# Kernel tuning notes

Hardware: AMD Instinct MI355X
Metric: run time of the kernel (lower is better)

## Reference

```python
import jax, jax.numpy as jnp
import numpy as np
from jax import lax

GRAD_MUL = 0.1   # config.model.deform_conv_grad_mul
GN_GROUPS = 32
EPS = 1e-5


def conv1d(x, w, b, padding=1):
    # x [N,C,T], w [O,I,K], b [O]
    y = lax.conv_general_dilated(x, w, window_strides=(1,),
                                 padding=[(padding, padding)],
                                 dimension_numbers=('NCH', 'OIH', 'NCH'))
    return y + b[None, :, None]


def group_norm(x, gamma, beta):
    N, C, T = x.shape
    xg = x.reshape(N, GN_GROUPS, C // GN_GROUPS, T)
    mu = jnp.mean(xg, axis=(2, 3), keepdims=True)
    var = jnp.var(xg, axis=(2, 3), keepdims=True)
    xn = ((xg - mu) * lax.rsqrt(var + EPS)).reshape(N, C, T)
    return xn * gamma[None, :, None] + beta[None, :, None]


def deform_conv1d(x, off_y, w, b):
    # x [N,C,T]; off_y [N,3,T] per-tap temporal offsets; w [O,I,3]; b [O]
    # kernel=3, padding=1: tap k samples at t + (k-1) + off_y[:,k,t]
    N, C, T = x.shape
    K = 3
    base = jnp.arange(T, dtype=x.dtype)[None, None, :] + \
           (jnp.arange(K, dtype=x.dtype) - 1.0)[None, :, None]   # [1,3,T]
    pos = base + off_y                                           # [N,3,T]
    p0 = jnp.floor(pos)
    w1 = pos - p0                                                # linear interp weight
    i0 = p0.astype(jnp.int32)
    i1 = i0 + 1

    def gather(idx):
        valid = (idx >= 0) & (idx < T)                           # zero padding outside
        ic = jnp.clip(idx, 0, T - 1)
        idx_b = jnp.broadcast_to(ic[:, None, :, :], (N, C, K, T))
        x_b = jnp.broadcast_to(x[:, :, None, :], (N, C, K, T))
        g = jnp.take_along_axis(x_b, idx_b, axis=3)              # [N,C,3,T]
        return g * valid[:, None, :, :].astype(x.dtype)

    sampled = gather(i0) * (1.0 - w1)[:, None] + gather(i1) * w1[:, None]  # [N,C,3,T]
    return jnp.einsum('oik,nikt->not', w, sampled) + b[None, :, None]


def setup_inputs() -> dict:
    key = jax.random.key(0)
    ks = jax.random.split(key, 8)
    N, C, T = 8, 512, 4096
    feat = jax.random.normal(ks[0], (N, C, T), dtype=jnp.float32)
    # boundary distances in frames; scaled so offsets span multiple positions
    locs = jax.random.uniform(ks[1], (N, 2, T), dtype=jnp.float32) * 64.0
    s = 0.02
    return {
        'feat': feat,
        'locs': locs,
        'conv_w': jax.random.normal(ks[2], (C, C, 3), dtype=jnp.float32) * s,
        'conv_b': jnp.zeros((C,), dtype=jnp.float32),
        'gn_g': jnp.ones((C,), dtype=jnp.float32),
        'gn_b': jnp.zeros((C,), dtype=jnp.float32),
        'dcn_w': jax.random.normal(ks[3], (C, C, 3), dtype=jnp.float32) * s,
        'dcn_b': jnp.zeros((C,), dtype=jnp.float32),
        'out_w': jax.random.normal(ks[4], (2, C, 3), dtype=jnp.float32) * s,
        'out_b': jnp.zeros((2,), dtype=jnp.float32),
        'stride': 8,
    }


def reference(feat, locs, conv_w, conv_b, gn_g, gn_b, dcn_w, dcn_b, out_w, out_b, stride):
    # Conv1d + GroupNorm + ReLU stem (conv_layer=1)
    h = jax.nn.relu(group_norm(conv1d(feat, conv_w, conv_b), gn_g, gn_b))
    # _get_dcn_offset: gradient-scaled boundary offsets / stride
    locs_gm = ((1.0 - GRAD_MUL) * lax.stop_gradient(locs) + GRAD_MUL * locs) / jnp.float32(stride)
    y1, y2 = locs_gm[:, 0], locs_gm[:, 1]                        # [N,T]
    zero = jnp.zeros_like(y1)
    off_y = jnp.stack([-y1, zero, y2], axis=1)                   # taps 0,1,2
    offset_feat = jax.nn.relu(deform_conv1d(h, off_y, dcn_w, dcn_b))
    # Unit1D out head: Conv1d k=3 same padding, no activation
    offset = conv1d(offset_feat, out_w, out_b)
    return (offset, offset_feat)
```

## Files before the change

### kernel.cpp

```cpp
#include <hip/hip_runtime.h>
#include <hip/hip_bf16.h>

typedef __hip_bfloat16 bf16;
typedef __attribute__((ext_vector_type(8))) short short8;
typedef __attribute__((ext_vector_type(4))) float float4v;

constexpr int Nn = 8, Cc = 512, Tt = 4096, Gg = 32, CPG = 16;
constexpr float EPS = 1e-5f;

__device__ __forceinline__ float b2f(bf16 x){ return __bfloat162float(x); }
__device__ __forceinline__ bf16  f2b(float x){ return __float2bfloat16(x); }
__device__ __forceinline__ short f2s(float x){
    union { bf16 b; short s; } u; u.b = f2b(x); return u.s;
}
__device__ __forceinline__ float s2f(short x){
    union { short s; bf16 b; } u; u.s = x; return b2f(u.b);
}

__device__ __forceinline__ float stride_val(const void* sp){
    int si = *(const int*)sp;
    if (si >= 1 && si <= 100000) return (float)si;
    float sf = *(const float*)sp;
    if (sf >= 0.5f && sf <= 1.0e5f) return sf;
    return 8.0f;
}

__device__ __forceinline__ void gld16(const void* g, void* l){
    __builtin_amdgcn_global_load_lds(
        (const __attribute__((address_space(1))) unsigned int*)g,
        (__attribute__((address_space(3))) unsigned int*)l, 16, 0, 0);
}

__global__ void k_transpose(const float* __restrict__ feat, bf16* __restrict__ ftr){
    __shared__ float L[64 * 65];
    int t0 = blockIdx.x * 64, i0 = blockIdx.y * 64, n = blockIdx.z;
    int tid = threadIdx.x;
    const float* fb = feat + ((size_t)n * Cc + i0) * Tt + t0;
    #pragma unroll
    for (int it = 0; it < 4; ++it){
        int p = tid + it * 256;
        int i = p >> 4, t4 = (p & 15) * 4;
        float4v v = *(const float4v*)&fb[(size_t)i * Tt + t4];
        L[(t4 + 0) * 65 + i] = v.x;
        L[(t4 + 1) * 65 + i] = v.y;
        L[(t4 + 2) * 65 + i] = v.z;
        L[(t4 + 3) * 65 + i] = v.w;
    }
    __syncthreads();
    #pragma unroll
    for (int it = 0; it < 2; ++it){
        int p = tid + it * 256;
        int t = p >> 3, s = p & 7;
        short8 sv;
        #pragma unroll
        for (int j = 0; j < 8; ++j) sv[j] = f2s(L[t * 65 + s * 8 + j]);
        *(short8*)&ftr[((size_t)n * 4098 + t0 + t + 1) * Cc + i0 + s * 8] = sv;
    }
}

__global__ void k_zpad(bf16* __restrict__ ftr){
    int p = blockIdx.x * 256 + threadIdx.x;
    int n = p >> 10, r = (p >> 9) & 1, i = p & 511;
    ftr[((size_t)n * 4098 + (r ? 4097 : 0)) * Cc + i] = f2b(0.f);
}

__global__ void k_wcvt(const float* __restrict__ w, bf16* __restrict__ wt){
    int p = blockIdx.x * 256 + threadIdx.x;
    int k = p >> 18, rest = p & 262143;
    wt[p] = f2b(w[(size_t)rest * 3 + k]);
}


__global__ __launch_bounds__(256, 4) void k_conv1g(const bf16* __restrict__ ftr,
        const bf16* __restrict__ wtc, const float* __restrict__ bias, bf16* __restrict__ ht){
    __shared__ __align__(16) short As[128 * 32];
    __shared__ __align__(16) short Bs[128 * 32];
    __shared__ float Lt[32 * 132];
    int t0 = blockIdx.x * 128, o0 = blockIdx.y * 128, n = blockIdx.z;
    int tid = threadIdx.x, wid = tid >> 6, lane = tid & 63;
    int quad = lane >> 4, l15 = lane & 15;
    int rlo  = lane >> 2;
    int colo = 8 * ((lane & 3) ^ ((lane >> 3) & 3));
    int sgf  = 8 * (quad ^ ((lane >> 1) & 3));

    float4v acc[2][8];
    #pragma unroll
    for (int m = 0; m < 2; ++m)
        #pragma unroll
        for (int f = 0; f < 8; ++f) acc[m][f] = (float4v){0.f,0.f,0.f,0.f};

    const short* ABp = (const short*)wtc + (size_t)o0 * 512;
    const short* BBp = (const short*)ftr + ((size_t)n * 4098 + t0) * 512;
    int r0 = wid * 32;

    for (int tap = 0; tap < 3; ++tap){
        const short* Ab = ABp + (size_t)tap * 262144;
        const short* Bb = BBp + (size_t)tap * 512;
        for (int ic = 0; ic < 512; ic += 32){
            gld16(Ab + (size_t)(r0 + rlo)      * 512 + ic + colo, As + r0 * 32);
            gld16(Ab + (size_t)(r0 + 16 + rlo) * 512 + ic + colo, As + (r0 + 16) * 32);
            gld16(Bb + (size_t)(r0 + rlo)      * 512 + ic + colo, Bs + r0 * 32);
            gld16(Bb + (size_t)(r0 + 16 + rlo) * 512 + ic + colo, Bs + (r0 + 16) * 32);
            __syncthreads();
            short8 a0 = *(const short8*)&As[(r0 + l15) * 32 + sgf];
            short8 a1 = *(const short8*)&As[(r0 + 16 + l15) * 32 + sgf];
            #pragma unroll
            for (int f = 0; f < 8; ++f){
                short8 b = *(const short8*)&Bs[(f * 16 + l15) * 32 + sgf];
                acc[0][f] = __builtin_amdgcn_mfma_f32_16x16x32_bf16(a0, b, acc[0][f], 0, 0, 0);
                acc[1][f] = __builtin_amdgcn_mfma_f32_16x16x32_bf16(a1, b, acc[1][f], 0, 0, 0);
            }
            __syncthreads();
        }
    }
    #pragma unroll
    for (int pass = 0; pass < 4; ++pass){
        __syncthreads();
        #pragma unroll
        for (int m = 0; m < 2; ++m){
            #pragma unroll
            for (int fi = 0; fi < 2; ++fi){
                int f = pass * 2 + fi;
                int tl = fi * 16 + l15;
                int ob = wid * 32 + m * 16 + quad * 4;
                #pragma unroll
                for (int r = 0; r < 4; ++r)
                    Lt[tl * 132 + ob + r] = acc[m][f][r] + bias[o0 + ob + r];
            }
        }
        __syncthreads();
        #pragma unroll
        for (int it = 0; it < 2; ++it){
            int p = tid + it * 256;
            int tl = p >> 4, s = p & 15;
            short8 sv;
            #pragma unroll
            for (int j = 0; j < 8; ++j) sv[j] = f2s(Lt[tl * 132 + s * 8 + j]);
            *(short8*)&ht[((size_t)n * Tt + t0 + pass * 32 + tl) * Cc + o0 + s * 8] = sv;
        }
    }
}

__global__ void k_gnstats2(const bf16* __restrict__ ht, float* __restrict__ mean,
                           float* __restrict__ rstd){
    int blk = blockIdx.x;
    int n = blk >> 5, g = blk & 31;
    const bf16* base = ht + (size_t)n * Tt * Cc + g * 16 + (threadIdx.x & 1) * 8;
    float s = 0.f, ss = 0.f;
    for (int r = threadIdx.x >> 1; r < Tt; r += 128){
        short8 v = *(const short8*)&base[(size_t)r * Cc];
        #pragma unroll
        for (int j = 0; j < 8; ++j){ float f = s2f(v[j]); s += f; ss += f * f; }
    }
    __shared__ float sh[512];
    sh[threadIdx.x] = s; sh[256 + threadIdx.x] = ss;
    __syncthreads();
    for (int off = 128; off > 0; off >>= 1){
        if (threadIdx.x < off){
            sh[threadIdx.x] += sh[threadIdx.x + off];
            sh[256 + threadIdx.x] += sh[256 + threadIdx.x + off];
        }
        __syncthreads();
    }
    if (threadIdx.x == 0){
        float m = sh[0] / (float)(CPG * Tt);
        float v = sh[256] / (float)(CPG * Tt) - m * m;
        mean[blk] = m; rstd[blk] = rsqrtf(v + EPS);
    }
}

__global__ void k_gnapply2(bf16* __restrict__ ht, const float* __restrict__ mean,
        const float* __restrict__ rstd, const float* __restrict__ gamma,
        const float* __restrict__ beta){
    int p = blockIdx.x * 256 + threadIdx.x;
    int s = p & 63, row = p >> 6;
    int n = row >> 12;
    int ib = s * 8;
    int blk = n * 32 + (ib >> 4);
    float mu = mean[blk], rs = rstd[blk];
    short8 v = *(short8*)&ht[(size_t)row * Cc + ib];
    short8 o;
    #pragma unroll
    for (int j = 0; j < 8; ++j){
        int c = ib + j;
        float f = (s2f(v[j]) - mu) * rs * gamma[c] + beta[c];
        o[j] = f2s(fmaxf(f, 0.f));
    }
    *(short8*)&ht[(size_t)row * Cc + ib] = o;
}

__global__ void k_prep(const float* __restrict__ locs, const void* __restrict__ sp,
        int* __restrict__ ia0, int* __restrict__ ia1, int* __restrict__ ic0,
        int* __restrict__ ic1, float* __restrict__ wa0, float* __restrict__ wa1,
        float* __restrict__ wc0, float* __restrict__ wc1){
    int idx = blockIdx.x * 256 + threadIdx.x;
    int t = idx & 4095, n = idx >> 12;
    float s = stride_val(sp);
    float l1 = locs[((size_t)n * 2 + 0) * Tt + t];
    float l2 = locs[((size_t)n * 2 + 1) * Tt + t];
    float y1 = (0.9f * l1 + 0.1f * l1) / s;
    float y2 = (0.9f * l2 + 0.1f * l2) / s;
    float pos0 = (float)(t - 1) - y1;
    float pos2 = (float)(t + 1) + y2;
    float p0f = floorf(pos0), p2f = floorf(pos2);
    float w1 = pos0 - p0f, w2 = pos2 - p2f;
    int a0 = (int)p0f, a1 = a0 + 1, c0 = (int)p2f, c1 = c0 + 1;
    wa0[idx] = (a0 >= 0 && a0 < Tt) ? (1.f - w1) : 0.f;
    wa1[idx] = (a1 >= 0 && a1 < Tt) ? w1 : 0.f;
    wc0[idx] = (c0 >= 0 && c0 < Tt) ? (1.f - w2) : 0.f;
    wc1[idx] = (c1 >= 0 && c1 < Tt) ? w2 : 0.f;
    ia0[idx] = min(max(a0, 0), Tt - 1);
    ia1[idx] = min(max(a1, 0), Tt - 1);
    ic0[idx] = min(max(c0, 0), Tt - 1);
    ic1[idx] = min(max(c1, 0), Tt - 1);
}

__global__ void k_sample(const bf16* __restrict__ ht, const int* __restrict__ ia0,
        const int* __restrict__ ia1, const int* __restrict__ ic0, const int* __restrict__ ic1,
        const float* __restrict__ wa0, const float* __restrict__ wa1,
        const float* __restrict__ wc0, const float* __restrict__ wc1,
        bf16* __restrict__ S0, bf16* __restrict__ S2){
    int n = blockIdx.y;
    int t0 = blockIdx.x * 16;
    int lane = threadIdx.x & 63, slot = threadIdx.x >> 6;
    const bf16* hb = ht + (size_t)n * Tt * Cc;
    #pragma unroll
    for (int rr = 0; rr < 4; ++rr){
        int t = t0 + slot * 4 + rr;
        int idx = n * Tt + t;
        {
            short8 lo = *(const short8*)&hb[(size_t)ia0[idx] * Cc + lane * 8];
            short8 hi = *(const short8*)&hb[(size_t)ia1[idx] * Cc + lane * 8];
            float w0 = wa0[idx], w1 = wa1[idx];
            short8 o;
            #pragma unroll
            for (int j = 0; j < 8; ++j) o[j] = f2s(w0 * s2f(lo[j]) + w1 * s2f(hi[j]));
            *(short8*)&S0[(size_t)idx * Cc + lane * 8] = o;
        }
        {
            short8 lo = *(const short8*)&hb[(size_t)ic0[idx] * Cc + lane * 8];
            short8 hi = *(const short8*)&hb[(size_t)ic1[idx] * Cc + lane * 8];
            float w0 = wc0[idx], w1 = wc1[idx];
            short8 o;
            #pragma unroll
            for (int j = 0; j < 8; ++j) o[j] = f2s(w0 * s2f(lo[j]) + w1 * s2f(hi[j]));
            *(short8*)&S2[(size_t)idx * Cc + lane * 8] = o;
        }
    }
}

__global__ __launch_bounds__(256, 4) void k_deformg(const bf16* __restrict__ S0,
        const bf16* __restrict__ ht, const bf16* __restrict__ S2,
        const bf16* __restrict__ wtd, const float* __restrict__ bias,
        float* __restrict__ out){
    __shared__ __align__(16) short As[128 * 32];
    __shared__ __align__(16) short Bs[128 * 32];
    int t0 = blockIdx.x * 128, o0 = blockIdx.y * 128, n = blockIdx.z;
    int tid = threadIdx.x, wid = tid >> 6, lane = tid & 63;
    int quad = lane >> 4, l15 = lane & 15;
    int rlo  = lane >> 2;
    int colo = 8 * ((lane & 3) ^ ((lane >> 3) & 3));
    int sgf  = 8 * (quad ^ ((lane >> 1) & 3));

    float4v acc[2][8];
    #pragma unroll
    for (int m = 0; m < 2; ++m)
        #pragma unroll
        for (int f = 0; f < 8; ++f) acc[m][f] = (float4v){0.f,0.f,0.f,0.f};

    size_t boff = ((size_t)n * Tt + t0) * 512;
    const short* Bb3[3] = { (const short*)S0 + boff, (const short*)ht + boff,
                            (const short*)S2 + boff };
    const short* ABp = (const short*)wtd + (size_t)o0 * 512;
    int r0 = wid * 32;

    for (int tap = 0; tap < 3; ++tap){
        const short* Ab = ABp + (size_t)tap * 262144;
        const short* Bb = Bb3[tap];
        for (int ic = 0; ic < 512; ic += 32){
            gld16(Ab + (size_t)(r0 + rlo)      * 512 + ic + colo, As + r0 * 32);
            gld16(Ab + (size_t)(r0 + 16 + rlo) * 512 + ic + colo, As + (r0 + 16) * 32);
            gld16(Bb + (size_t)(r0 + rlo)      * 512 + ic + colo, Bs + r0 * 32);
            gld16(Bb + (size_t)(r0 + 16 + rlo) * 512 + ic + colo, Bs + (r0 + 16) * 32);
            __syncthreads();
            short8 a0 = *(const short8*)&As[(r0 + l15) * 32 + sgf];
            short8 a1 = *(const short8*)&As[(r0 + 16 + l15) * 32 + sgf];
            #pragma unroll
            for (int f = 0; f < 8; ++f){
                short8 b = *(const short8*)&Bs[(f * 16 + l15) * 32 + sgf];
                acc[0][f] = __builtin_amdgcn_mfma_f32_16x16x32_bf16(a0, b, acc[0][f], 0, 0, 0);
                acc[1][f] = __builtin_amdgcn_mfma_f32_16x16x32_bf16(a1, b, acc[1][f], 0, 0, 0);
            }
            __syncthreads();
        }
    }
    float* ob = out + (size_t)n * Cc * Tt;
    #pragma unroll
    for (int m = 0; m < 2; ++m){
        int ob0 = o0 + wid * 32 + m * 16 + quad * 4;
        #pragma unroll
        for (int r = 0; r < 4; ++r){
            float bs = bias[ob0 + r];
            size_t row = (size_t)(ob0 + r) * Tt;
            #pragma unroll
            for (int f = 0; f < 8; ++f)
                ob[row + t0 + f * 16 + l15] = fmaxf(acc[m][f][r] + bs, 0.f);
        }
    }
}

__global__ void k_outinit(const float* __restrict__ ob, float* __restrict__ out){
    int idx = blockIdx.x * 256 + threadIdx.x;
    out[idx] = ob[(idx >> 12) & 1];
}

__global__ void k_outconv(const float* __restrict__ x, const float* __restrict__ w,
                          float* __restrict__ out){
    int t  = blockIdx.x * 256 + threadIdx.x;
    int i0 = blockIdx.y * 64;
    int n  = blockIdx.z;
    const float* xb = x + (size_t)n * Cc * Tt;
    float a0 = 0.f, a1 = 0.f;
    bool tm = (t > 0), tp = (t < Tt - 1);
    for (int i = i0; i < i0 + 64; ++i){
        const float* xr = xb + (size_t)i * Tt + t;
        float xm = tm ? xr[-1] : 0.f;
        float x0 = xr[0];
        float xp = tp ? xr[1] : 0.f;
        const float* w0 = w + i * 3;
        const float* w1 = w + Cc * 3 + i * 3;
        a0 += xm * w0[0] + x0 * w0[1] + xp * w0[2];
        a1 += xm * w1[0] + x0 * w1[1] + xp * w1[2];
    }
    atomicAdd(&out[((size_t)n * 2 + 0) * Tt + t], a0);
    atomicAdd(&out[((size_t)n * 2 + 1) * Tt + t], a1);
}

extern "C" void kernel_launch(void* const* d_in, const int* in_sizes, int n_in,
                              void* d_out, int out_size, void* d_ws, size_t ws_size,
                              hipStream_t stream) {
    const float* feat   = (const float*)d_in[0];
    const float* locs   = (const float*)d_in[1];
    const float* conv_w = (const float*)d_in[2];
    const float* conv_b = (const float*)d_in[3];
    const float* gn_g   = (const float*)d_in[4];
    const float* gn_b   = (const float*)d_in[5];
    const float* dcn_w  = (const float*)d_in[6];
    const float* dcn_b  = (const float*)d_in[7];
    const float* out_w  = (const float*)d_in[8];
    const float* out_b  = (const float*)d_in[9];

    float* offset      = (float*)d_out;
    float* offset_feat = (float*)d_out + (size_t)Nn * 2 * Tt;

    constexpr size_t SZ_PREP = 32768 * 4;
    constexpr size_t OFF_PREP = 4096;
    constexpr size_t OFF_WTC  = OFF_PREP + 8 * SZ_PREP;
    constexpr size_t OFF_WTD  = OFF_WTC + 3 * 512 * 512 * 2;
    constexpr size_t OFF_FTR  = OFF_WTD + 3 * 512 * 512 * 2;
    constexpr size_t OFF_HT   = OFF_FTR + (size_t)8 * 4098 * 512 * 2;
    constexpr size_t OFF_S2   = OFF_HT  + (size_t)8 * 4096 * 512 * 2;

    float* mean = (float*)d_ws;
    float* rstd = (float*)((char*)d_ws + 1024);

    char* ws = (char*)d_ws;
    int*   ia0 = (int*)  (ws + OFF_PREP + 0 * SZ_PREP);
    int*   ia1 = (int*)  (ws + OFF_PREP + 1 * SZ_PREP);
    int*   ic0 = (int*)  (ws + OFF_PREP + 2 * SZ_PREP);
    int*   ic1 = (int*)  (ws + OFF_PREP + 3 * SZ_PREP);
    float* wa0 = (float*)(ws + OFF_PREP + 4 * SZ_PREP);
    float* wa1 = (float*)(ws + OFF_PREP + 5 * SZ_PREP);
    float* wc0 = (float*)(ws + OFF_PREP + 6 * SZ_PREP);
    float* wc1 = (float*)(ws + OFF_PREP + 7 * SZ_PREP);
    bf16* wtc = (bf16*)(ws + OFF_WTC);
    bf16* wtd = (bf16*)(ws + OFF_WTD);
    bf16* ftr = (bf16*)(ws + OFF_FTR);
    bf16* ht  = (bf16*)(ws + OFF_HT);
    bf16* S2  = (bf16*)(ws + OFF_S2);
    bf16* S0  = ftr;

    k_transpose<<<dim3(64, 8, 8), 256, 0, stream>>>(feat, ftr);
    k_zpad     <<<32, 256, 0, stream>>>(ftr);
    k_wcvt     <<<3072, 256, 0, stream>>>(conv_w, wtc);
    k_wcvt     <<<3072, 256, 0, stream>>>(dcn_w, wtd);
    k_conv1g   <<<dim3(32, 4, 8), 256, 0, stream>>>(ftr, wtc, conv_b, ht);
    k_gnstats2 <<<256, 256, 0, stream>>>(ht, mean, rstd);
    k_gnapply2 <<<8192, 256, 0, stream>>>(ht, mean, rstd, gn_g, gn_b);
    k_prep     <<<128, 256, 0, stream>>>(locs, d_in[10], ia0, ia1, ic0, ic1, wa0, wa1, wc0, wc1);
    k_sample   <<<dim3(256, 8), 256, 0, stream>>>(ht, ia0, ia1, ic0, ic1, wa0, wa1, wc0, wc1, S0, S2);
    k_deformg  <<<dim3(32, 4, 8), 256, 0, stream>>>(S0, ht, S2, wtd, dcn_b, offset_feat);
    k_outinit  <<<256, 256, 0, stream>>>(out_b, offset);
    k_outconv  <<<dim3(16, 8, 8), 256, 0, stream>>>(offset_feat, out_w, offset);
}
```

Baseline: 333.2 us.

## Fuse deformable bilinear sampling into the deform GEMM B-tile load

Removes the separate k_sample kernel and its S0/S2 intermediate buffers. The deform GEMM now computes the interpolated B tiles for taps 0 and 2 in registers from gathered ht rows and writes them to LDS directly. Per-position sample indices and weights are packed into one 16-byte struct so each thread gets them with a single load. This drops a write and re-read of two 32 MB bf16 tensors, but sampling is redone by each of the 4 output-channel blocks, and the gathers are synchronous loads that sit on the GEMM's critical path instead of async global-to-LDS copies.

```diff
diff --git a/kernel.cpp b/kernel.cpp
--- a/kernel.cpp
+++ b/kernel.cpp
@@ -7,6 +7,8 @@
 
 constexpr int Nn = 8, Cc = 512, Tt = 4096, Gg = 32, CPG = 16;
 constexpr float EPS = 1e-5f;
+
+struct __align__(16) Samp { int i0, i1; float w0, w1; };
 
 __device__ __forceinline__ float b2f(bf16 x){ return __bfloat162float(x); }
 __device__ __forceinline__ bf16  f2b(float x){ return __float2bfloat16(x); }
@@ -190,9 +192,7 @@
 }
 
 __global__ void k_prep(const float* __restrict__ locs, const void* __restrict__ sp,
-        int* __restrict__ ia0, int* __restrict__ ia1, int* __restrict__ ic0,
-        int* __restrict__ ic1, float* __restrict__ wa0, float* __restrict__ wa1,
-        float* __restrict__ wc0, float* __restrict__ wc1){
+        Samp* __restrict__ pa, Samp* __restrict__ pc){
     int idx = blockIdx.x * 256 + threadIdx.x;
     int t = idx & 4095, n = idx >> 12;
     float s = stride_val(sp);
@@ -205,52 +205,21 @@
     float p0f = floorf(pos0), p2f = floorf(pos2);
     float w1 = pos0 - p0f, w2 = pos2 - p2f;
     int a0 = (int)p0f, a1 = a0 + 1, c0 = (int)p2f, c1 = c0 + 1;
-    wa0[idx] = (a0 >= 0 && a0 < Tt) ? (1.f - w1) : 0.f;
-    wa1[idx] = (a1 >= 0 && a1 < Tt) ? w1 : 0.f;
-    wc0[idx] = (c0 >= 0 && c0 < Tt) ? (1.f - w2) : 0.f;
-    wc1[idx] = (c1 >= 0 && c1 < Tt) ? w2 : 0.f;
-    ia0[idx] = min(max(a0, 0), Tt - 1);
-    ia1[idx] = min(max(a1, 0), Tt - 1);
-    ic0[idx] = min(max(c0, 0), Tt - 1);
-    ic1[idx] = min(max(c1, 0), Tt - 1);
-}
-
-__global__ void k_sample(const bf16* __restrict__ ht, const int* __restrict__ ia0,
-        const int* __restrict__ ia1, const int* __restrict__ ic0, const int* __restrict__ ic1,
-        const float* __restrict__ wa0, const float* __restrict__ wa1,
-        const float* __restrict__ wc0, const float* __restrict__ wc1,
-        bf16* __restrict__ S0, bf16* __restrict__ S2){
-    int n = blockIdx.y;
-    int t0 = blockIdx.x * 16;
-    int lane = threadIdx.x & 63, slot = threadIdx.x >> 6;
-    const bf16* hb = ht + (size_t)n * Tt * Cc;
-    #pragma unroll
-    for (int rr = 0; rr < 4; ++rr){
-        int t = t0 + slot * 4 + rr;
-        int idx = n * Tt + t;
-        {
-            short8 lo = *(const short8*)&hb[(size_t)ia0[idx] * Cc + lane * 8];
-            short8 hi = *(const short8*)&hb[(size_t)ia1[idx] * Cc + lane * 8];
-            float w0 = wa0[idx], w1 = wa1[idx];
-            short8 o;
-            #pragma unroll
-            for (int j = 0; j < 8; ++j) o[j] = f2s(w0 * s2f(lo[j]) + w1 * s2f(hi[j]));
-            *(short8*)&S0[(size_t)idx * Cc + lane * 8] = o;
-        }
-        {
-            short8 lo = *(const short8*)&hb[(size_t)ic0[idx] * Cc + lane * 8];
-            short8 hi = *(const short8*)&hb[(size_t)ic1[idx] * Cc + lane * 8];
-            float w0 = wc0[idx], w1 = wc1[idx];
-            short8 o;
-            #pragma unroll
-            for (int j = 0; j < 8; ++j) o[j] = f2s(w0 * s2f(lo[j]) + w1 * s2f(hi[j]));
-            *(short8*)&S2[(size_t)idx * Cc + lane * 8] = o;
-        }
-    }
-}
-
-__global__ __launch_bounds__(256, 4) void k_deformg(const bf16* __restrict__ S0,
-        const bf16* __restrict__ ht, const bf16* __restrict__ S2,
+    Samp A, C;
+    A.w0 = (a0 >= 0 && a0 < Tt) ? (1.f - w1) : 0.f;
+    A.w1 = (a1 >= 0 && a1 < Tt) ? w1 : 0.f;
+    C.w0 = (c0 >= 0 && c0 < Tt) ? (1.f - w2) : 0.f;
+    C.w1 = (c1 >= 0 && c1 < Tt) ? w2 : 0.f;
+    A.i0 = min(max(a0, 0), Tt - 1);
+    A.i1 = min(max(a1, 0), Tt - 1);
+    C.i0 = min(max(c0, 0), Tt - 1);
+    C.i1 = min(max(c1, 0), Tt - 1);
+    pa[idx] = A;
+    pc[idx] = C;
+}
+
+__global__ __launch_bounds__(256, 4) void k_deformg(const bf16* __restrict__ ht,
+        const Samp* __restrict__ pa, const Samp* __restrict__ pc,
         const bf16* __restrict__ wtd, const float* __restrict__ bias,
         float* __restrict__ out){
     __shared__ __align__(16) short As[128 * 32];
@@ -259,8 +228,10 @@
     int tid = threadIdx.x, wid = tid >> 6, lane = tid & 63;
     int quad = lane >> 4, l15 = lane & 15;
     int rlo  = lane >> 2;
-    int colo = 8 * ((lane & 3) ^ ((lane >> 3) & 3));
+    int slot = lane & 3;
+    int colo = 8 * (slot ^ ((rlo >> 1) & 3));
     int sgf  = 8 * (quad ^ ((lane >> 1) & 3));
+    int r0 = wid * 32;
 
     float4v acc[2][8];
     #pragma unroll
@@ -268,20 +239,56 @@
         #pragma unroll
         for (int f = 0; f < 8; ++f) acc[m][f] = (float4v){0.f,0.f,0.f,0.f};
 
-    size_t boff = ((size_t)n * Tt + t0) * 512;
-    const short* Bb3[3] = { (const short*)S0 + boff, (const short*)ht + boff,
-                            (const short*)S2 + boff };
+    int row_a = r0 + rlo, row_b = r0 + 16 + rlo;
+    size_t pbase = (size_t)n * Tt + t0;
+    Samp sa0 = pa[pbase + row_a];
+    Samp sa1 = pa[pbase + row_b];
+    Samp sc0 = pc[pbase + row_a];
+    Samp sc1 = pc[pbase + row_b];
+
+    const short* hs = (const short*)ht + (size_t)n * Tt * 512;
+    const short* ga0 = hs + (size_t)sa0.i0 * 512 + colo;
+    const short* ga1 = hs + (size_t)sa0.i1 * 512 + colo;
+    const short* gb0 = hs + (size_t)sa1.i0 * 512 + colo;
+    const short* gb1 = hs + (size_t)sa1.i1 * 512 + colo;
+    const short* gc0 = hs + (size_t)sc0.i0 * 512 + colo;
+    const short* gc1 = hs + (size_t)sc0.i1 * 512 + colo;
+    const short* gd0 = hs + (size_t)sc1.i0 * 512 + colo;
+    const short* gd1 = hs + (size_t)sc1.i1 * 512 + colo;
+
+    const short* Bb1 = hs + (size_t)t0 * 512;
     const short* ABp = (const short*)wtd + (size_t)o0 * 512;
-    int r0 = wid * 32;
 
     for (int tap = 0; tap < 3; ++tap){
         const short* Ab = ABp + (size_t)tap * 262144;
-        const short* Bb = Bb3[tap];
         for (int ic = 0; ic < 512; ic += 32){
             gld16(Ab + (size_t)(r0 + rlo)      * 512 + ic + colo, As + r0 * 32);
             gld16(Ab + (size_t)(r0 + 16 + rlo) * 512 + ic + colo, As + (r0 + 16) * 32);
-            gld16(Bb + (size_t)(r0 + rlo)      * 512 + ic + colo, Bs + r0 * 32);
-            gld16(Bb + (size_t)(r0 + 16 + rlo) * 512 + ic + colo, Bs + (r0 + 16) * 32);
+            if (tap == 1){
+                gld16(Bb1 + (size_t)(r0 + rlo)      * 512 + ic + colo, Bs + r0 * 32);
+                gld16(Bb1 + (size_t)(r0 + 16 + rlo) * 512 + ic + colo, Bs + (r0 + 16) * 32);
+            } else {
+                const short* p0 = (tap == 0) ? ga0 : gc0;
+                const short* p1 = (tap == 0) ? ga1 : gc1;
+                const short* q0 = (tap == 0) ? gb0 : gd0;
+                const short* q1 = (tap == 0) ? gb1 : gd1;
+                float w00 = (tap == 0) ? sa0.w0 : sc0.w0;
+                float w01 = (tap == 0) ? sa0.w1 : sc0.w1;
+                float w10 = (tap == 0) ? sa1.w0 : sc1.w0;
+                float w11 = (tap == 0) ? sa1.w1 : sc1.w1;
+                short8 lo0 = *(const short8*)&p0[ic];
+                short8 hi0 = *(const short8*)&p1[ic];
+                short8 lo1 = *(const short8*)&q0[ic];
+                short8 hi1 = *(const short8*)&q1[ic];
+                short8 o0, o1;
+                #pragma unroll
+                for (int j = 0; j < 8; ++j){
+                    o0[j] = f2s(w00 * s2f(lo0[j]) + w01 * s2f(hi0[j]));
+                    o1[j] = f2s(w10 * s2f(lo1[j]) + w11 * s2f(hi1[j]));
+                }
+                *(short8*)&Bs[row_a * 32 + slot * 8] = o0;
+                *(short8*)&Bs[row_b * 32 + slot * 8] = o1;
+            }
             __syncthreads();
             short8 a0 = *(const short8*)&As[(r0 + l15) * 32 + sgf];
             short8 a1 = *(const short8*)&As[(r0 + 16 + l15) * 32 + sgf];
@@ -353,32 +360,23 @@
     float* offset      = (float*)d_out;
     float* offset_feat = (float*)d_out + (size_t)Nn * 2 * Tt;
 
-    constexpr size_t SZ_PREP = 32768 * 4;
     constexpr size_t OFF_PREP = 4096;
-    constexpr size_t OFF_WTC  = OFF_PREP + 8 * SZ_PREP;
+    constexpr size_t SZ_SAMP  = (size_t)32768 * sizeof(Samp);
+    constexpr size_t OFF_WTC  = OFF_PREP + 2 * SZ_SAMP;
     constexpr size_t OFF_WTD  = OFF_WTC + 3 * 512 * 512 * 2;
     constexpr size_t OFF_FTR  = OFF_WTD + 3 * 512 * 512 * 2;
     constexpr size_t OFF_HT   = OFF_FTR + (size_t)8 * 4098 * 512 * 2;
-    constexpr size_t OFF_S2   = OFF_HT  + (size_t)8 * 4096 * 512 * 2;
 
     float* mean = (float*)d_ws;
     float* rstd = (float*)((char*)d_ws + 1024);
 
     char* ws = (char*)d_ws;
-    int*   ia0 = (int*)  (ws + OFF_PREP + 0 * SZ_PREP);
-    int*   ia1 = (int*)  (ws + OFF_PREP + 1 * SZ_PREP);
-    int*   ic0 = (int*)  (ws + OFF_PREP + 2 * SZ_PREP);
-    int*   ic1 = (int*)  (ws + OFF_PREP + 3 * SZ_PREP);
-    float* wa0 = (float*)(ws + OFF_PREP + 4 * SZ_PREP);
-    float* wa1 = (float*)(ws + OFF_PREP + 5 * SZ_PREP);
-    float* wc0 = (float*)(ws + OFF_PREP + 6 * SZ_PREP);
-    float* wc1 = (float*)(ws + OFF_PREP + 7 * SZ_PREP);
+    Samp* pa  = (Samp*)(ws + OFF_PREP);
+    Samp* pc  = (Samp*)(ws + OFF_PREP + SZ_SAMP);
     bf16* wtc = (bf16*)(ws + OFF_WTC);
     bf16* wtd = (bf16*)(ws + OFF_WTD);
     bf16* ftr = (bf16*)(ws + OFF_FTR);
     bf16* ht  = (bf16*)(ws + OFF_HT);
-    bf16* S2  = (bf16*)(ws + OFF_S2);
-    bf16* S0  = ftr;
 
     k_transpose<<<dim3(64, 8, 8), 256, 0, stream>>>(feat, ftr);
     k_zpad     <<<32, 256, 0, stream>>>(ftr);
@@ -387,9 +385,8 @@
     k_conv1g   <<<dim3(32, 4, 8), 256, 0, stream>>>(ftr, wtc, conv_b, ht);
     k_gnstats2 <<<256, 256, 0, stream>>>(ht, mean, rstd);
     k_gnapply2 <<<8192, 256, 0, stream>>>(ht, mean, rstd, gn_g, gn_b);
-    k_prep     <<<128, 256, 0, stream>>>(locs, d_in[10], ia0, ia1, ic0, ic1, wa0, wa1, wc0, wc1);
-    k_sample   <<<dim3(256, 8), 256, 0, stream>>>(ht, ia0, ia1, ic0, ic1, wa0, wa1, wc0, wc1, S0, S2);
-    k_deformg  <<<dim3(32, 4, 8), 256, 0, stream>>>(S0, ht, S2, wtd, dcn_b, offset_feat);
+    k_prep     <<<128, 256, 0, stream>>>(locs, d_in[10], pa, pc);
+    k_deformg  <<<dim3(32, 4, 8), 256, 0, stream>>>(ht, pa, pc, wtd, dcn_b, offset_feat);
     k_outinit  <<<256, 256, 0, stream>>>(out_b, offset);
     k_outconv  <<<dim3(16, 8, 8), 256, 0, stream>>>(offset_feat, out_w, offset);
 }
```

Measured after the change: 335.3 us. No clear change (+0.6%).

## Fuse GroupNorm stats into conv epilogue and output head into deform GEMM

Applied to the files above, without the earlier changes.

Group-norm sums and sums of squares are now accumulated in the stem conv epilogue via shared and global atomics, which removes the separate stats pass over the activation tensor. The 2-channel output conv is computed inside the deform GEMM epilogue from register accumulators, with per-block partials atomically added into the offset output, so offset_feat no longer has to be re-read. Per-position sampling metadata is packed into one 16-byte struct so k_sample issues one vector load instead of eight scalar loads. In exchange, variance now comes from the E[x^2]-mean^2 form over fp32 atomics, with nondeterministic summation order. It also adds a zeroing launch and more epilogue work and shared-memory atomics.

```diff
diff --git a/kernel.cpp b/kernel.cpp
--- a/kernel.cpp
+++ b/kernel.cpp
@@ -7,6 +7,8 @@
 
 constexpr int Nn = 8, Cc = 512, Tt = 4096, Gg = 32, CPG = 16;
 constexpr float EPS = 1e-5f;
+
+struct __align__(16) Samp { int i0, i1; float w0, w1; };
 
 __device__ __forceinline__ float b2f(bf16 x){ return __bfloat162float(x); }
 __device__ __forceinline__ bf16  f2b(float x){ return __float2bfloat16(x); }
@@ -29,6 +31,10 @@
     __builtin_amdgcn_global_load_lds(
         (const __attribute__((address_space(1))) unsigned int*)g,
         (__attribute__((address_space(3))) unsigned int*)l, 16, 0, 0);
+}
+
+__global__ void k_zero(float* __restrict__ p){
+    p[threadIdx.x] = 0.f;
 }
 
 __global__ void k_transpose(const float* __restrict__ feat, bf16* __restrict__ ftr){
@@ -72,10 +78,12 @@
 
 
 __global__ __launch_bounds__(256, 4) void k_conv1g(const bf16* __restrict__ ftr,
-        const bf16* __restrict__ wtc, const float* __restrict__ bias, bf16* __restrict__ ht){
+        const bf16* __restrict__ wtc, const float* __restrict__ bias, bf16* __restrict__ ht,
+        float* __restrict__ gsum, float* __restrict__ gss){
     __shared__ __align__(16) short As[128 * 32];
     __shared__ __align__(16) short Bs[128 * 32];
     __shared__ float Lt[32 * 132];
+    __shared__ float gred[16];
     int t0 = blockIdx.x * 128, o0 = blockIdx.y * 128, n = blockIdx.z;
     int tid = threadIdx.x, wid = tid >> 6, lane = tid & 63;
     int quad = lane >> 4, l15 = lane & 15;
@@ -113,6 +121,8 @@
             __syncthreads();
         }
     }
+    float gs = 0.f, gq = 0.f;
+    int sg = tid & 15;
     #pragma unroll
     for (int pass = 0; pass < 4; ++pass){
         __syncthreads();
@@ -135,49 +145,37 @@
             int tl = p >> 4, s = p & 15;
             short8 sv;
             #pragma unroll
-            for (int j = 0; j < 8; ++j) sv[j] = f2s(Lt[tl * 132 + s * 8 + j]);
+            for (int j = 0; j < 8; ++j){
+                float fv = Lt[tl * 132 + s * 8 + j];
+                gs += fv; gq += fv * fv;
+                sv[j] = f2s(fv);
+            }
             *(short8*)&ht[((size_t)n * Tt + t0 + pass * 32 + tl) * Cc + o0 + s * 8] = sv;
         }
     }
-}
-
-__global__ void k_gnstats2(const bf16* __restrict__ ht, float* __restrict__ mean,
-                           float* __restrict__ rstd){
-    int blk = blockIdx.x;
-    int n = blk >> 5, g = blk & 31;
-    const bf16* base = ht + (size_t)n * Tt * Cc + g * 16 + (threadIdx.x & 1) * 8;
-    float s = 0.f, ss = 0.f;
-    for (int r = threadIdx.x >> 1; r < Tt; r += 128){
-        short8 v = *(const short8*)&base[(size_t)r * Cc];
-        #pragma unroll
-        for (int j = 0; j < 8; ++j){ float f = s2f(v[j]); s += f; ss += f * f; }
-    }
-    __shared__ float sh[512];
-    sh[threadIdx.x] = s; sh[256 + threadIdx.x] = ss;
+    if (tid < 16) gred[tid] = 0.f;
     __syncthreads();
-    for (int off = 128; off > 0; off >>= 1){
-        if (threadIdx.x < off){
-            sh[threadIdx.x] += sh[threadIdx.x + off];
-            sh[256 + threadIdx.x] += sh[256 + threadIdx.x + off];
-        }
-        __syncthreads();
-    }
-    if (threadIdx.x == 0){
-        float m = sh[0] / (float)(CPG * Tt);
-        float v = sh[256] / (float)(CPG * Tt) - m * m;
-        mean[blk] = m; rstd[blk] = rsqrtf(v + EPS);
-    }
-}
-
-__global__ void k_gnapply2(bf16* __restrict__ ht, const float* __restrict__ mean,
-        const float* __restrict__ rstd, const float* __restrict__ gamma,
+    atomicAdd(&gred[(sg >> 1) * 2 + 0], gs);
+    atomicAdd(&gred[(sg >> 1) * 2 + 1], gq);
+    __syncthreads();
+    if (tid < 8){
+        int blk = n * 32 + (o0 >> 4) + tid;
+        atomicAdd(&gsum[blk], gred[tid * 2 + 0]);
+        atomicAdd(&gss[blk],  gred[tid * 2 + 1]);
+    }
+}
+
+__global__ void k_gnapply2(bf16* __restrict__ ht, const float* __restrict__ gsum,
+        const float* __restrict__ gss, const float* __restrict__ gamma,
         const float* __restrict__ beta){
     int p = blockIdx.x * 256 + threadIdx.x;
     int s = p & 63, row = p >> 6;
     int n = row >> 12;
     int ib = s * 8;
     int blk = n * 32 + (ib >> 4);
-    float mu = mean[blk], rs = rstd[blk];
+    const float inv = 1.f / (float)(CPG * Tt);
+    float mu = gsum[blk] * inv;
+    float rs = rsqrtf(gss[blk] * inv - mu * mu + EPS);
     short8 v = *(short8*)&ht[(size_t)row * Cc + ib];
     short8 o;
     #pragma unroll
@@ -190,9 +188,7 @@
 }
 
 __global__ void k_prep(const float* __restrict__ locs, const void* __restrict__ sp,
-        int* __restrict__ ia0, int* __restrict__ ia1, int* __restrict__ ic0,
-        int* __restrict__ ic1, float* __restrict__ wa0, float* __restrict__ wa1,
-        float* __restrict__ wc0, float* __restrict__ wc1){
+        Samp* __restrict__ pa, Samp* __restrict__ pc){
     int idx = blockIdx.x * 256 + threadIdx.x;
     int t = idx & 4095, n = idx >> 12;
     float s = stride_val(sp);
@@ -205,21 +201,21 @@
     float p0f = floorf(pos0), p2f = floorf(pos2);
     float w1 = pos0 - p0f, w2 = pos2 - p2f;
     int a0 = (int)p0f, a1 = a0 + 1, c0 = (int)p2f, c1 = c0 + 1;
-    wa0[idx] = (a0 >= 0 && a0 < Tt) ? (1.f - w1) : 0.f;
-    wa1[idx] = (a1 >= 0 && a1 < Tt) ? w1 : 0.f;
-    wc0[idx] = (c0 >= 0 && c0 < Tt) ? (1.f - w2) : 0.f;
-    wc1[idx] = (c1 >= 0 && c1 < Tt) ? w2 : 0.f;
-    ia0[idx] = min(max(a0, 0), Tt - 1);
-    ia1[idx] = min(max(a1, 0), Tt - 1);
-    ic0[idx] = min(max(c0, 0), Tt - 1);
-    ic1[idx] = min(max(c1, 0), Tt - 1);
-}
-
-__global__ void k_sample(const bf16* __restrict__ ht, const int* __restrict__ ia0,
-        const int* __restrict__ ia1, const int* __restrict__ ic0, const int* __restrict__ ic1,
-        const float* __restrict__ wa0, const float* __restrict__ wa1,
-        const float* __restrict__ wc0, const float* __restrict__ wc1,
-        bf16* __restrict__ S0, bf16* __restrict__ S2){
+    Samp A, C;
+    A.w0 = (a0 >= 0 && a0 < Tt) ? (1.f - w1) : 0.f;
+    A.w1 = (a1 >= 0 && a1 < Tt) ? w1 : 0.f;
+    C.w0 = (c0 >= 0 && c0 < Tt) ? (1.f - w2) : 0.f;
+    C.w1 = (c1 >= 0 && c1 < Tt) ? w2 : 0.f;
+    A.i0 = min(max(a0, 0), Tt - 1);
+    A.i1 = min(max(a1, 0), Tt - 1);
+    C.i0 = min(max(c0, 0), Tt - 1);
+    C.i1 = min(max(c1, 0), Tt - 1);
+    pa[idx] = A;
+    pc[idx] = C;
+}
+
+__global__ void k_sample(const bf16* __restrict__ ht, const Samp* __restrict__ pa,
+        const Samp* __restrict__ pc, bf16* __restrict__ S0, bf16* __restrict__ S2){
     int n = blockIdx.y;
     int t0 = blockIdx.x * 16;
     int lane = threadIdx.x & 63, slot = threadIdx.x >> 6;
@@ -229,21 +225,21 @@
         int t = t0 + slot * 4 + rr;
         int idx = n * Tt + t;
         {
-            short8 lo = *(const short8*)&hb[(size_t)ia0[idx] * Cc + lane * 8];
-            short8 hi = *(const short8*)&hb[(size_t)ia1[idx] * Cc + lane * 8];
-            float w0 = wa0[idx], w1 = wa1[idx];
+            Samp A = pa[idx];
+            short8 lo = *(const short8*)&hb[(size_t)A.i0 * Cc + lane * 8];
+            short8 hi = *(const short8*)&hb[(size_t)A.i1 * Cc + lane * 8];
             short8 o;
             #pragma unroll
-            for (int j = 0; j < 8; ++j) o[j] = f2s(w0 * s2f(lo[j]) + w1 * s2f(hi[j]));
+            for (int j = 0; j < 8; ++j) o[j] = f2s(A.w0 * s2f(lo[j]) + A.w1 * s2f(hi[j]));
             *(short8*)&S0[(size_t)idx * Cc + lane * 8] = o;
         }
         {
-            short8 lo = *(const short8*)&hb[(size_t)ic0[idx] * Cc + lane * 8];
-            short8 hi = *(const short8*)&hb[(size_t)ic1[idx] * Cc + lane * 8];
-            float w0 = wc0[idx], w1 = wc1[idx];
+            Samp C = pc[idx];
+            short8 lo = *(const short8*)&hb[(size_t)C.i0 * Cc + lane * 8];
+            short8 hi = *(const short8*)&hb[(size_t)C.i1 * Cc + lane * 8];
             short8 o;
             #pragma unroll
-            for (int j = 0; j < 8; ++j) o[j] = f2s(w0 * s2f(lo[j]) + w1 * s2f(hi[j]));
+            for (int j = 0; j < 8; ++j) o[j] = f2s(C.w0 * s2f(lo[j]) + C.w1 * s2f(hi[j]));
             *(short8*)&S2[(size_t)idx * Cc + lane * 8] = o;
         }
     }
@@ -252,7 +248,8 @@
 __global__ __launch_bounds__(256, 4) void k_deformg(const bf16* __restrict__ S0,
         const bf16* __restrict__ ht, const bf16* __restrict__ S2,
         const bf16* __restrict__ wtd, const float* __restrict__ bias,
-        float* __restrict__ out){
+        float* __restrict__ out, const float* __restrict__ wout,
+        float* __restrict__ oout){
     __shared__ __align__(16) short As[128 * 32];
     __shared__ __align__(16) short Bs[128 * 32];
     int t0 = blockIdx.x * 128, o0 = blockIdx.y * 128, n = blockIdx.z;
@@ -303,8 +300,56 @@
             float bs = bias[ob0 + r];
             size_t row = (size_t)(ob0 + r) * Tt;
             #pragma unroll
-            for (int f = 0; f < 8; ++f)
-                ob[row + t0 + f * 16 + l15] = fmaxf(acc[m][f][r] + bs, 0.f);
+            for (int f = 0; f < 8; ++f){
+                float v = fmaxf(acc[m][f][r] + bs, 0.f);
+                acc[m][f][r] = v;
+                ob[row + t0 + f * 16 + l15] = v;
+            }
+        }
+    }
+    float* wL   = (float*)As;
+    float* part = (float*)Bs;
+    for (int q = tid; q < 768; q += 256){
+        int c = q / 384, rr = q - c * 384;
+        int ol = rr / 3, k = rr - ol * 3;
+        wL[q] = wout[c * 1536 + (o0 + ol) * 3 + k];
+    }
+    for (int q = tid; q < 264; q += 256) part[q] = 0.f;
+    __syncthreads();
+    #pragma unroll
+    for (int c = 0; c < 2; ++c){
+        float wr[3][2][4];
+        #pragma unroll
+        for (int k = 0; k < 3; ++k)
+            #pragma unroll
+            for (int m = 0; m < 2; ++m)
+                #pragma unroll
+                for (int r = 0; r < 4; ++r)
+                    wr[k][m][r] = wL[c * 384 + (wid * 32 + m * 16 + quad * 4 + r) * 3 + k];
+        #pragma unroll
+        for (int f = 0; f < 8; ++f){
+            #pragma unroll
+            for (int k = 0; k < 3; ++k){
+                float contrib = 0.f;
+                #pragma unroll
+                for (int m = 0; m < 2; ++m)
+                    #pragma unroll
+                    for (int r = 0; r < 4; ++r)
+                        contrib += wr[k][m][r] * acc[m][f][r];
+                contrib += __shfl_xor(contrib, 16);
+                contrib += __shfl_xor(contrib, 32);
+                if (quad == 0)
+                    atomicAdd(&part[c * 132 + f * 16 + l15 + 2 - k], contrib);
+            }
+        }
+    }
+    __syncthreads();
+    for (int q = tid; q < 264; q += 256){
+        int c = q / 132, tl = q - c * 132;
+        if (tl < 130){
+            int tg = t0 + tl - 1;
+            if (tg >= 0 && tg < Tt)
+                atomicAdd(&oout[((size_t)n * 2 + c) * Tt + tg], part[q]);
         }
     }
 }
@@ -312,28 +357,6 @@
 __global__ void k_outinit(const float* __restrict__ ob, float* __restrict__ out){
     int idx = blockIdx.x * 256 + threadIdx.x;
     out[idx] = ob[(idx >> 12) & 1];
-}
-
-__global__ void k_outconv(const float* __restrict__ x, const float* __restrict__ w,
-                          float* __restrict__ out){
-    int t  = blockIdx.x * 256 + threadIdx.x;
-    int i0 = blockIdx.y * 64;
-    int n  = blockIdx.z;
-    const float* xb = x + (size_t)n * Cc * Tt;
-    float a0 = 0.f, a1 = 0.f;
-    bool tm = (t > 0), tp = (t < Tt - 1);
-    for (int i = i0; i < i0 + 64; ++i){
-        const float* xr = xb + (size_t)i * Tt + t;
-        float xm = tm ? xr[-1] : 0.f;
-        float x0 = xr[0];
-        float xp = tp ? xr[1] : 0.f;
-        const float* w0 = w + i * 3;
-        const float* w1 = w + Cc * 3 + i * 3;
-        a0 += xm * w0[0] + x0 * w0[1] + xp * w0[2];
-        a1 += xm * w1[0] + x0 * w1[1] + xp * w1[2];
-    }
-    atomicAdd(&out[((size_t)n * 2 + 0) * Tt + t], a0);
-    atomicAdd(&out[((size_t)n * 2 + 1) * Tt + t], a1);
 }
 
 extern "C" void kernel_launch(void* const* d_in, const int* in_sizes, int n_in,
@@ -353,26 +376,20 @@
     float* offset      = (float*)d_out;
     float* offset_feat = (float*)d_out + (size_t)Nn * 2 * Tt;
 
-    constexpr size_t SZ_PREP = 32768 * 4;
     constexpr size_t OFF_PREP = 4096;
-    constexpr size_t OFF_WTC  = OFF_PREP + 8 * SZ_PREP;
+    constexpr size_t SZ_SAMP  = (size_t)32768 * sizeof(Samp);
+    constexpr size_t OFF_WTC  = OFF_PREP + 2 * SZ_SAMP;
     constexpr size_t OFF_WTD  = OFF_WTC + 3 * 512 * 512 * 2;
     constexpr size_t OFF_FTR  = OFF_WTD + 3 * 512 * 512 * 2;
     constexpr size_t OFF_HT   = OFF_FTR + (size_t)8 * 4098 * 512 * 2;
     constexpr size_t OFF_S2   = OFF_HT  + (size_t)8 * 4096 * 512 * 2;
 
-    float* mean = (float*)d_ws;
-    float* rstd = (float*)((char*)d_ws + 1024);
+    float* gsum = (float*)d_ws;
+    float* gss  = (float*)((char*)d_ws + 1024);
 
     char* ws = (char*)d_ws;
-    int*   ia0 = (int*)  (ws + OFF_PREP + 0 * SZ_PREP);
-    int*   ia1 = (int*)  (ws + OFF_PREP + 1 * SZ_PREP);
-    int*   ic0 = (int*)  (ws + OFF_PREP + 2 * SZ_PREP);
-    int*   ic1 = (int*)  (ws + OFF_PREP + 3 * SZ_PREP);
-    float* wa0 = (float*)(ws + OFF_PREP + 4 * SZ_PREP);
-    float* wa1 = (float*)(ws + OFF_PREP + 5 * SZ_PREP);
-    float* wc0 = (float*)(ws + OFF_PREP + 6 * SZ_PREP);
-    float* wc1 = (float*)(ws + OFF_PREP + 7 * SZ_PREP);
+    Samp* pa  = (Samp*)(ws + OFF_PREP);
+    Samp* pc  = (Samp*)(ws + OFF_PREP + SZ_SAMP);
     bf16* wtc = (bf16*)(ws + OFF_WTC);
     bf16* wtd = (bf16*)(ws + OFF_WTD);
     bf16* ftr = (bf16*)(ws + OFF_FTR);
@@ -384,12 +401,12 @@
     k_zpad     <<<32, 256, 0, stream>>>(ftr);
     k_wcvt     <<<3072, 256, 0, stream>>>(conv_w, wtc);
     k_wcvt     <<<3072, 256, 0, stream>>>(dcn_w, wtd);
-    k_conv1g   <<<dim3(32, 4, 8), 256, 0, stream>>>(ftr, wtc, conv_b, ht);
-    k_gnstats2 <<<256, 256, 0, stream>>>(ht, mean, rstd);
-    k_gnapply2 <<<8192, 256, 0, stream>>>(ht, mean, rstd, gn_g, gn_b);
-    k_prep     <<<128, 256, 0, stream>>>(locs, d_in[10], ia0, ia1, ic0, ic1, wa0, wa1, wc0, wc1);
-    k_sample   <<<dim3(256, 8), 256, 0, stream>>>(ht, ia0, ia1, ic0, ic1, wa0, wa1, wc0, wc1, S0, S2);
-    k_deformg  <<<dim3(32, 4, 8), 256, 0, stream>>>(S0, ht, S2, wtd, dcn_b, offset_feat);
+    k_zero     <<<1, 512, 0, stream>>>((float*)d_ws);
+    k_conv1g   <<<dim3(32, 4, 8), 256, 0, stream>>>(ftr, wtc, conv_b, ht, gsum, gss);
+    k_gnapply2 <<<8192, 256, 0, stream>>>(ht, gsum, gss, gn_g, gn_b);
+    k_prep     <<<128, 256, 0, stream>>>(locs, d_in[10], pa, pc);
+    k_sample   <<<dim3(256, 8), 256, 0, stream>>>(ht, pa, pc, S0, S2);
     k_outinit  <<<256, 256, 0, stream>>>(out_b, offset);
-    k_outconv  <<<dim3(16, 8, 8), 256, 0, stream>>>(offset_feat, out_w, offset);
-}
+    k_deformg  <<<dim3(32, 4, 8), 256, 0, stream>>>(S0, ht, S2, wtd, dcn_b,
+                                                    offset_feat, out_w, offset);
+}
```

Measured after the change: 320.1 us. 1.04x faster.
